# Performance work log

Hardware: AMD Instinct MI355X
Metric: run time of the kernel (lower is better)

Reference implementation:

```python
import jax, jax.numpy as jnp
import numpy as np

B, N, F, D, H, S_OBJ, S_REG, ITERS = 32, 1024, 1152, 512, 8, 8, 4, 3
S = S_OBJ + S_REG
HD = D // H
SCALE = HD ** -0.5


def ln(x, g, b, eps=1e-5):
    m = x.mean(-1, keepdims=True)
    v = ((x - m) ** 2).mean(-1, keepdims=True)
    return (x - m) / jnp.sqrt(v + eps) * g + b


def setup_inputs() -> dict:
    key = jax.random.key(0)
    ks = jax.random.split(key, 16)
    s = 0.02
    d = {
        'features': jax.random.normal(ks[0], (B, N, F), jnp.float32),
        'noise': jax.random.normal(ks[1], (B, S, D), jnp.float32),
        'w_in': jax.random.normal(ks[2], (F, D), jnp.float32) * s,
        'b_in': jnp.zeros((D,), jnp.float32),
        'ln1_g': jnp.ones((D,), jnp.float32), 'ln1_b': jnp.zeros((D,), jnp.float32),
        'slot_mu': jax.random.normal(ks[3], (1, S, D), jnp.float32) * D ** -0.5,
        'slot_log_sigma': jnp.zeros((1, S, D), jnp.float32),
        'wq': jax.random.normal(ks[4], (D, D), jnp.float32) * s,
        'wk': jax.random.normal(ks[5], (D, D), jnp.float32) * s,
        'wv': jax.random.normal(ks[6], (D, D), jnp.float32) * s,
        'gru_wih': jax.random.normal(ks[7], (D, 3 * D), jnp.float32) * s,
        'gru_whh': jax.random.normal(ks[8], (D, 3 * D), jnp.float32) * s,
        'gru_bih': jnp.zeros((3 * D,), jnp.float32),
        'gru_bhh': jnp.zeros((3 * D,), jnp.float32),
        'nslots_g': jnp.ones((D,), jnp.float32), 'nslots_b': jnp.zeros((D,), jnp.float32),
        'ninput_g': jnp.ones((D,), jnp.float32), 'ninput_b': jnp.zeros((D,), jnp.float32),
        'ffn_ln_g': jnp.ones((D,), jnp.float32), 'ffn_ln_b': jnp.zeros((D,), jnp.float32),
        'ffn_w1': jax.random.normal(ks[9], (D, 4 * D), jnp.float32) * s,
        'ffn_b1': jnp.zeros((4 * D,), jnp.float32),
        'ffn_w2': jax.random.normal(ks[10], (4 * D, D), jnp.float32) * s,
        'ffn_b2': jnp.zeros((D,), jnp.float32),
        'sel_w1': jax.random.normal(ks[11], (D, D // 2), jnp.float32) * s,
        'sel_b1': jnp.zeros((D // 2,), jnp.float32),
        'sel_w2': jax.random.normal(ks[12], (D // 2, 2), jnp.float32) * s,
        'sel_b2': jnp.zeros((2,), jnp.float32),
    }
    return d


def reference(features, noise, w_in, b_in, ln1_g, ln1_b, slot_mu, slot_log_sigma,
              wq, wk, wv, gru_wih, gru_whh, gru_bih, gru_bhh,
              nslots_g, nslots_b, ninput_g, ninput_b,
              ffn_ln_g, ffn_ln_b, ffn_w1, ffn_b1, ffn_w2, ffn_b2,
              sel_w1, sel_b1, sel_w2, sel_b2):
    b = features.shape[0]
    # input_proj: Linear + LayerNorm, then norm_input LayerNorm
    x = ln(features @ w_in + b_in, ln1_g, ln1_b)
    inp = ln(x, ninput_g, ninput_b)
    slots = slot_mu + jnp.exp(slot_log_sigma) * noise  # [B,S,D]
    k = (inp @ wk).reshape(b, N, H, HD)
    v = (inp @ wv).reshape(b, N, H, HD)
    attn_out = None
    for _ in range(ITERS):
        sn = ln(slots, nslots_g, nslots_b)
        q = (sn @ wq).reshape(b, S, H, HD)
        dots = jnp.einsum('bihd,bjhd->bihj', q, k) * SCALE  # [B,S,H,N]
        # softmax over flattened (slot, head) axis per key j
        attn = jax.nn.softmax(dots.reshape(b, S * H, N), axis=1).reshape(b, S, H, N)
        attn_out = attn.mean(axis=2)  # [B,S,N]
        attn_n = (attn + 1e-8) / (attn.sum(axis=-1, keepdims=True) + 1e-8)
        upd = jnp.einsum('bjhd,bihj->bihd', v, attn_n).reshape(b * S, D)
        h = slots.reshape(b * S, D)
        gx = upd @ gru_wih + gru_bih
        gh = h @ gru_whh + gru_bhh
        xr, xz, xn = jnp.split(gx, 3, axis=-1)
        hr, hz, hn = jnp.split(gh, 3, axis=-1)
        r = jax.nn.sigmoid(xr + hr)
        z = jax.nn.sigmoid(xz + hz)
        n = jnp.tanh(xn + r * hn)
        slots = ((1.0 - z) * n + z * h).reshape(b, S, D)
        f = ln(slots, ffn_ln_g, ffn_ln_b)
        f = jax.nn.gelu(f @ ffn_w1 + ffn_b1, approximate=False) @ ffn_w2 + ffn_b2
        slots = slots + f
    obj = slots[:, :S_OBJ]  # [B,num_slots,D]
    logits = jax.nn.relu(obj @ sel_w1 + sel_b1) @ sel_w2 + sel_b2  # [B,num_slots,2]
    decision = (jnp.argmax(logits, axis=-1) == 1).astype(slots.dtype)
    # eval-mode repair: ensure >=2 active slots per row (deterministic: first inactive)
    needed = jnp.maximum(0.0, 2.0 - decision.sum(-1, keepdims=True))
    inactive_rank = jnp.cumsum(1.0 - decision, axis=-1)
    add = ((decision == 0) & (inactive_rank <= needed)).astype(decision.dtype)
    decision = decision + add
    obj = obj * decision[..., None]
    return obj, decision, attn_out[:, :S_OBJ]
```

## Files before the change

### kernel.cpp

```cpp
#include <hip/hip_runtime.h>
#include <math.h>

typedef __attribute__((ext_vector_type(8))) short short8;
typedef __attribute__((ext_vector_type(4))) float f32x4;

typedef const __attribute__((address_space(1))) void gv_t;
typedef __attribute__((address_space(3))) void lv_t;

__device__ __forceinline__ float b2f(short u) {
  union { unsigned int i; float f; } c; c.i = ((unsigned int)(unsigned short)u) << 16; return c.f;
}
__device__ __forceinline__ short f2b(float f) {
  union { float f; unsigned int i; } c; c.f = f;
  unsigned int r = c.i + 0x7FFFu + ((c.i >> 16) & 1u);
  return (short)(r >> 16);
}
__device__ __forceinline__ void glds(const short* g, short* l) {
  __builtin_amdgcn_global_load_lds((gv_t*)g, (lv_t*)l, 16, 0, 0);
}


__global__ __launch_bounds__(256) void k_convA(const float* __restrict__ in, short* __restrict__ out, int n8) {
  int idx = blockIdx.x * 256 + threadIdx.x;
  if (idx >= n8) return;
  const float4* p = (const float4*)(in + (size_t)idx * 8);
  float4 a = p[0], b = p[1];
  short8 r;
  r[0]=f2b(a.x); r[1]=f2b(a.y); r[2]=f2b(a.z); r[3]=f2b(a.w);
  r[4]=f2b(b.x); r[5]=f2b(b.y); r[6]=f2b(b.z); r[7]=f2b(b.w);
  *(short8*)(out + (size_t)idx*8) = r;
}


__global__ __launch_bounds__(256) void k_prep(
    const float* __restrict__ w_in, const float* __restrict__ wk, const float* __restrict__ wv,
    const float* __restrict__ wq, const float* __restrict__ wih, const float* __restrict__ whh,
    const float* __restrict__ bih, const float* __restrict__ bhh,
    const float* __restrict__ w1, const float* __restrict__ w2, const float* __restrict__ sl1,
    const float* __restrict__ mu, const float* __restrict__ lsig, const float* __restrict__ noise,
    short* __restrict__ Bt1, short* __restrict__ Btkv, short* __restrict__ wq_t,
    short* __restrict__ wgru, float* __restrict__ gbias,
    short* __restrict__ w1_t, short* __restrict__ w2_t, short* __restrict__ sl1_t,
    float* __restrict__ slots, short* __restrict__ gruA)
{
  int blk = blockIdx.x, t = threadIdx.x;
  if (blk < 2304) {
    int idx = blk*256 + t;
    int kk = idx / 512, n = idx % 512;
    Bt1[(size_t)n*1152 + kk] = f2b(w_in[idx]);
  } else if (blk < 4352) {
    int idx = (blk-2304)*256 + t;
    int kk = idx >> 10, n = idx & 1023;
    float v = (n < 512) ? wk[kk*512 + n] : wv[kk*512 + (n-512)];
    Btkv[(size_t)n*512 + kk] = f2b(v);
  } else if (blk < 5376) {
    int idx = (blk-4352)*256 + t;
    int kk = idx >> 9, n = idx & 511;
    wq_t[n*512 + kk] = f2b(wq[idx]);
  } else if (blk < 13568) {
    int idx = (blk-5376)*256 + t;
    int n = idx >> 10, k = idx & 1023;
    int g = n >> 9, c = n & 511;
    float v;
    if (g == 0)      v = (k < 512) ? wih[k*1536 + c]        : whh[(k-512)*1536 + c];
    else if (g == 1) v = (k < 512) ? wih[k*1536 + 512 + c]  : whh[(k-512)*1536 + 512 + c];
    else if (g == 2) v = (k < 512) ? wih[k*1536 + 1024 + c] : 0.f;
    else             v = (k < 512) ? 0.f                    : whh[(k-512)*1536 + 1024 + c];
    wgru[(size_t)n*1024 + k] = f2b(v);
  } else if (blk < 17664) {
    int idx = (blk-13568)*256 + t;
    int kk = idx >> 11, n = idx & 2047;
    w1_t[(size_t)n*512 + kk] = f2b(w1[idx]);
  } else if (blk < 21760) {
    int idx = (blk-17664)*256 + t;
    int kk = idx >> 9, n = idx & 511;
    w2_t[(size_t)n*2048 + kk] = f2b(w2[idx]);
  } else if (blk < 22272) {
    int idx = (blk-21760)*256 + t;
    int kk = idx >> 8, n = idx & 255;
    sl1_t[n*512 + kk] = f2b(sl1[idx]);
  } else if (blk < 22280) {
    int n = (blk-22272)*256 + t;
    int g = n >> 9;
    float v;
    if (g <= 1)      v = bih[n] + bhh[n];
    else if (g == 2) v = bih[n];
    else             v = bhh[1024 + (n - 1536)];
    gbias[n] = v;
  } else {
    int idx = (blk-22280)*256 + t;
    int sd = idx % 6144;
    float v = mu[sd] + __expf(lsig[sd]) * noise[idx];
    slots[idx] = v;
    int row = idx >> 9, c = idx & 511;
    gruA[(size_t)row*1024 + 512 + c] = f2b(v);
  }
}


__global__ __launch_bounds__(256) void gemm_p(
    const short* __restrict__ A, const short* __restrict__ Bt,
    const float* __restrict__ bias, short* __restrict__ Cb,
    int N, int K, int lda, int ldb)
{
  __shared__ short As[2][128*64];
  __shared__ short Bs[2][128*64];
  const int t = threadIdx.x;
  const int lane = t & 63, wave = t >> 6;

  const int nwg = gridDim.x, gridX = N >> 7, orig = blockIdx.x;
  const int q = nwg >> 3, r = nwg & 7, xcd = orig & 7, base = orig >> 3;
  const int wgid = (xcd < r ? xcd*(q+1) : r*(q+1) + (xcd - r)*q) + base;
  const int bx = wgid % gridX, by = wgid / gridX;

  const int rowBase = by * 128, colBase = bx * 128;
  const int wm = (wave >> 1) * 64, wn = (wave & 1) * 64;
  const int fr = lane & 15, kcf = lane >> 4;
  f32x4 acc[4][4] = {};

  int srow[4], scol[4];
  #pragma unroll
  for (int i = 0; i < 4; ++i) {
    int c = i*256 + t;
    srow[i] = c >> 3;
    scol[i] = ((c & 7) ^ (srow[i] & 7)) * 8;
  }

  const int nsteps = K >> 6;
  auto STAGE = [&](int step, int buf) {
    int kb = step * 64;
    #pragma unroll
    for (int i = 0; i < 4; ++i) {
      int c = i*256 + t;
      glds(A + (size_t)(rowBase + srow[i])*lda + kb + scol[i], As[buf] + c*8);
      glds(Bt + (size_t)(colBase + srow[i])*ldb + kb + scol[i], Bs[buf] + c*8);
    }
  };

  STAGE(0, 0);
  if (nsteps > 1) { STAGE(1, 1); asm volatile("s_waitcnt vmcnt(8)" ::: "memory"); }
  else            {              asm volatile("s_waitcnt vmcnt(0)" ::: "memory"); }
  __builtin_amdgcn_sched_barrier(0);
  __builtin_amdgcn_s_barrier();
  __builtin_amdgcn_sched_barrier(0);

  for (int tt = 0; tt < nsteps; ++tt) {
    const int cur = tt & 1;
    short8 af[2][4], bf[2][4];
    #pragma unroll
    for (int ks = 0; ks < 2; ++ks) {
      int kc = ks*4 + kcf;
      #pragma unroll
      for (int m = 0; m < 4; ++m) {
        int rowa = wm + m*16 + fr;
        af[ks][m] = *(const short8*)(As[cur] + rowa*64 + (kc ^ (rowa & 7))*8);
        int rowb = wn + m*16 + fr;
        bf[ks][m] = *(const short8*)(Bs[cur] + rowb*64 + (kc ^ (rowb & 7))*8);
      }
    }
    asm volatile("s_waitcnt lgkmcnt(0)" ::: "memory");
    __builtin_amdgcn_sched_barrier(0);
    __builtin_amdgcn_s_barrier();
    __builtin_amdgcn_sched_barrier(0);
    if (tt + 2 < nsteps) STAGE(tt + 2, cur);
    #pragma unroll
    for (int ks = 0; ks < 2; ++ks)
      #pragma unroll
      for (int m = 0; m < 4; ++m)
        #pragma unroll
        for (int n = 0; n < 4; ++n)
          acc[m][n] = __builtin_amdgcn_mfma_f32_16x16x32_bf16(af[ks][m], bf[ks][n], acc[m][n], 0, 0, 0);
    if (tt + 1 < nsteps) {
      if (tt + 2 < nsteps) asm volatile("s_waitcnt vmcnt(8)" ::: "memory");
      else                 asm volatile("s_waitcnt vmcnt(0)" ::: "memory");
      __builtin_amdgcn_sched_barrier(0);
      __builtin_amdgcn_s_barrier();
      __builtin_amdgcn_sched_barrier(0);
    }
  }

  const int cr = (lane >> 4) * 4, cc2 = lane & 15;
  #pragma unroll
  for (int m = 0; m < 4; ++m)
    #pragma unroll
    for (int n = 0; n < 4; ++n) {
      int col = colBase + wn + n*16 + cc2;
      float bv = bias ? bias[col] : 0.f;
      #pragma unroll
      for (int j = 0; j < 4; ++j) {
        int row = rowBase + wm + m*16 + cr + j;
        Cb[(size_t)row*N + col] = f2b(acc[m][n][j] + bv);
      }
    }
}


template<int ACT, bool OUTBF, bool SPLITK>
__global__ __launch_bounds__(256) void gemm_t(
    const short* __restrict__ A, const short* __restrict__ Bt,
    const float* __restrict__ bias,
    float* __restrict__ Cf, short* __restrict__ Cb,
    int N, int Kp, int lda, int ldb, int ldf, int ldcb, int cboff, int skstride)
{
  __shared__ short As[128*64];
  __shared__ short Bs[128*64];
  const int t = threadIdx.x;
  const int lane = t & 63, wave = t >> 6;

  const int nwg = gridDim.x, gridX = N >> 7, orig = blockIdx.x;
  const int q = nwg >> 3, r = nwg & 7, xcd = orig & 7, base = orig >> 3;
  const int wgid = (xcd < r ? xcd*(q+1) : r*(q+1) + (xcd - r)*q) + base;
  const int bx = wgid % gridX, by = wgid / gridX;

  const int rowBase = by * 128, colBase = bx * 128;
  const size_t koff = (size_t)blockIdx.y * Kp;
  const int wm = (wave >> 1) * 64, wn = (wave & 1) * 64;
  const int fr = lane & 15, kcf = lane >> 4;
  f32x4 acc[4][4] = {};

  int srow[4], scol[4];
  #pragma unroll
  for (int i = 0; i < 4; ++i) {
    int c = i*256 + t;
    srow[i] = c >> 3;
    scol[i] = ((c & 7) ^ (srow[i] & 7)) * 8;
  }

  for (int kb = 0; kb < Kp; kb += 64) {
    __syncthreads();
    #pragma unroll
    for (int i = 0; i < 4; ++i) {
      int c = i*256 + t;
      glds(A + (size_t)(rowBase + srow[i])*lda + koff + kb + scol[i], As + c*8);
      glds(Bt + (size_t)(colBase + srow[i])*ldb + koff + kb + scol[i], Bs + c*8);
    }
    __syncthreads();
    #pragma unroll
    for (int ks = 0; ks < 2; ++ks) {
      short8 af[4], bf[4];
      #pragma unroll
      for (int m = 0; m < 4; ++m) {
        int row = wm + m*16 + fr;
        int kc = ks*4 + kcf;
        af[m] = *(const short8*)(As + row*64 + (kc ^ (row & 7))*8);
      }
      #pragma unroll
      for (int n = 0; n < 4; ++n) {
        int row = wn + n*16 + fr;
        int kc = ks*4 + kcf;
        bf[n] = *(const short8*)(Bs + row*64 + (kc ^ (row & 7))*8);
      }
      #pragma unroll
      for (int m = 0; m < 4; ++m)
        #pragma unroll
        for (int n = 0; n < 4; ++n)
          acc[m][n] = __builtin_amdgcn_mfma_f32_16x16x32_bf16(af[m], bf[n], acc[m][n], 0, 0, 0);
    }
  }

  const int cr = (lane >> 4) * 4, cc2 = lane & 15;
  if (SPLITK) {
    float* dst = Cf + (size_t)blockIdx.y * skstride;
    #pragma unroll
    for (int m = 0; m < 4; ++m)
      #pragma unroll
      for (int n = 0; n < 4; ++n) {
        int col = colBase + wn + n*16 + cc2;
        #pragma unroll
        for (int j = 0; j < 4; ++j) {
          int row = rowBase + wm + m*16 + cr + j;
          dst[(size_t)row * ldf + col] = acc[m][n][j];
        }
      }
  } else {
    #pragma unroll
    for (int m = 0; m < 4; ++m)
      #pragma unroll
      for (int n = 0; n < 4; ++n) {
        int col = colBase + wn + n*16 + cc2;
        float bv = bias ? bias[col] : 0.f;
        #pragma unroll
        for (int j = 0; j < 4; ++j) {
          int row = rowBase + wm + m*16 + cr + j;
          float v = acc[m][n][j] + bv;
          if (ACT == 1) v = 0.5f*v*(1.f + erff(v*0.70710678118f));
          else if (ACT == 2) v = fmaxf(v, 0.f);
          if (OUTBF) Cb[(size_t)row*ldcb + cboff + col] = f2b(v);
          else Cf[(size_t)row*ldf + col] = v;
        }
      }
  }
}


__global__ __launch_bounds__(256) void k_gruact_sk(const float* __restrict__ p, const float* __restrict__ gbias,
                                                   float* __restrict__ slots)
{
  int idx = blockIdx.x*256 + threadIdx.x;
  int row = idx >> 9, c = idx & 511;
  const float* base = p + (size_t)row*2048 + c;
  float g0=gbias[c], g1=gbias[512+c], g2=gbias[1024+c], g3=gbias[1536+c];
  #pragma unroll
  for (int s = 0; s < 4; ++s) {
    const float* qq = base + (size_t)s*786432;
    g0 += qq[0]; g1 += qq[512]; g2 += qq[1024]; g3 += qq[1536];
  }
  float r = 1.f/(1.f+__expf(-g0));
  float z = 1.f/(1.f+__expf(-g1));
  float n = tanhf(g2 + r*g3);
  slots[idx] = (1.f-z)*n + z*slots[idx];
}

__global__ __launch_bounds__(256) void k_ffn1red(const float* __restrict__ p, const float* __restrict__ b1,
                                                 short* __restrict__ f1) {
  int i = blockIdx.x*256 + threadIdx.x;
  int col = (i*8) & 2047;
  float v[8], w[8];
  *(float4*)v = *(const float4*)(p + (size_t)i*8);
  *(float4*)(v+4) = *(const float4*)(p + (size_t)i*8 + 4);
  const float* p2 = p + 786432;
  *(float4*)w = *(const float4*)(p2 + (size_t)i*8);
  *(float4*)(w+4) = *(const float4*)(p2 + (size_t)i*8 + 4);
  short8 o;
  #pragma unroll
  for (int e = 0; e < 8; ++e) {
    float x = v[e] + w[e] + b1[col + e];
    x = 0.5f*x*(1.f + erff(x*0.70710678118f));
    o[e] = f2b(x);
  }
  *(short8*)(f1 + (size_t)i*8) = o;
}

__global__ __launch_bounds__(256) void k_ffn2red(const float* __restrict__ p, const float* __restrict__ b2,
                                                 float* __restrict__ slots, short* __restrict__ gruA) {
  int i = blockIdx.x*256 + threadIdx.x;
  int base = i*8;
  int row = base >> 9, c = base & 511;
  float v[8] = {0.f,0.f,0.f,0.f,0.f,0.f,0.f,0.f};
  #pragma unroll
  for (int s = 0; s < 8; ++s) {
    const float* qq = p + (size_t)s*196608 + base;
    float4 a = *(const float4*)qq, b = *(const float4*)(qq+4);
    v[0]+=a.x; v[1]+=a.y; v[2]+=a.z; v[3]+=a.w;
    v[4]+=b.x; v[5]+=b.y; v[6]+=b.z; v[7]+=b.w;
  }
  float sl[8];
  *(float4*)sl = *(const float4*)(slots + base);
  *(float4*)(sl+4) = *(const float4*)(slots + base + 4);
  short8 o;
  #pragma unroll
  for (int e = 0; e < 8; ++e) {
    float ns = sl[e] + v[e] + b2[c+e];
    sl[e] = ns;
    o[e] = f2b(ns);
  }
  *(float4*)(slots + base) = *(float4*)sl;
  *(float4*)(slots + base + 4) = *(float4*)(sl+4);
  *(short8*)(gruA + (size_t)row*1024 + 512 + c) = o;
}


__global__ __launch_bounds__(256) void k_ln2(const short* __restrict__ y, short* __restrict__ inp,
    const float* __restrict__ g1, const float* __restrict__ b1,
    const float* __restrict__ g2, const float* __restrict__ b2)
{
  int t = threadIdx.x, lane = t & 63;
  int row = blockIdx.x * 4 + (t >> 6);
  const short8 raw = *(const short8*)(y + (size_t)row*512 + lane*8);
  float x[8];
  #pragma unroll
  for (int e = 0; e < 8; ++e) x[e] = b2f(raw[e]);
  float s = 0.f, ss = 0.f;
  #pragma unroll
  for (int e = 0; e < 8; ++e) { s += x[e]; ss += x[e]*x[e]; }
  #pragma unroll
  for (int m = 1; m < 64; m <<= 1) { s += __shfl_xor(s, m, 64); ss += __shfl_xor(ss, m, 64); }
  float mean = s * (1.f/512.f);
  float rs = rsqrtf(ss*(1.f/512.f) - mean*mean + 1e-5f);
  int c = lane * 8;
  #pragma unroll
  for (int e = 0; e < 8; ++e) x[e] = (x[e]-mean)*rs*g1[c+e] + b1[c+e];
  s = 0.f; ss = 0.f;
  #pragma unroll
  for (int e = 0; e < 8; ++e) { s += x[e]; ss += x[e]*x[e]; }
  #pragma unroll
  for (int m = 1; m < 64; m <<= 1) { s += __shfl_xor(s, m, 64); ss += __shfl_xor(ss, m, 64); }
  float mean2 = s * (1.f/512.f);
  float rs2 = rsqrtf(ss*(1.f/512.f) - mean2*mean2 + 1e-5f);
  short8 o;
  #pragma unroll
  for (int e = 0; e < 8; ++e) o[e] = f2b((x[e]-mean2)*rs2*g2[c+e] + b2[c+e]);
  *(short8*)(inp + (size_t)row*512 + lane*8) = o;
}


__global__ __launch_bounds__(256) void k_lnb(const float* __restrict__ x, short* __restrict__ out,
    const float* __restrict__ g, const float* __restrict__ b)
{
  int t = threadIdx.x, lane = t & 63;
  int row = blockIdx.x * 4 + (t >> 6);
  const float* src = x + (size_t)row*512 + lane*8;
  float v[8];
  *(float4*)v = *(const float4*)src;
  *(float4*)(v+4) = *(const float4*)(src+4);
  float s = 0.f, ss = 0.f;
  #pragma unroll
  for (int e = 0; e < 8; ++e) { s += v[e]; ss += v[e]*v[e]; }
  #pragma unroll
  for (int m = 1; m < 64; m <<= 1) { s += __shfl_xor(s, m, 64); ss += __shfl_xor(ss, m, 64); }
  float mean = s * (1.f/512.f);
  float rs = rsqrtf(ss*(1.f/512.f) - mean*mean + 1e-5f);
  int c = lane * 8;
  short8 o;
  #pragma unroll
  for (int e = 0; e < 8; ++e) o[e] = f2b((v[e]-mean)*rs*g[c+e] + b[c+e]);
  *(short8*)(out + (size_t)row*512 + c) = o;
}


__global__ __launch_bounds__(256) void k_attn(
    const float* __restrict__ qparts, const short* __restrict__ kv,
    float* __restrict__ pvp, float* __restrict__ denp, float* __restrict__ aout)
{
  __shared__ float qs[12][512];
  __shared__ float ksh[128][65];
  __shared__ float dots[96][132];
  const int t = threadIdx.x;
  const int jt = blockIdx.x, b = blockIdx.y;

  for (int i = t; i < 6144; i += 256) {
    int s = i >> 9, d = i & 511;
    size_t o = (size_t)(b*12+s)*512 + d;
    qs[s][d] = qparts[o] + qparts[196608 + o] + qparts[393216 + o] + qparts[589824 + o];
  }

  const int jj = t & 127, sg = t >> 7;
  for (int h = 0; h < 8; ++h) {
    __syncthreads();
    #pragma unroll
    for (int i = 0; i < 4; ++i) {
      int c = i*256 + t;
      int j2 = c >> 3, seg = (c & 7) * 8;
      short8 raw = *(const short8*)(kv + ((size_t)(b*1024 + jt*128 + j2))*1024 + h*64 + seg);
      #pragma unroll
      for (int e = 0; e < 8; ++e) ksh[j2][seg+e] = b2f(raw[e]);
    }
    __syncthreads();
    float d6[6] = {};
    for (int d = 0; d < 64; ++d) {
      float kvv = ksh[jj][d];
      #pragma unroll
      for (int i = 0; i < 6; ++i) d6[i] += qs[sg*6+i][h*64+d] * kvv;
    }
    #pragma unroll
    for (int i = 0; i < 6; ++i) dots[(sg*6+i)*8 + h][jj] = d6[i] * 0.125f;
  }
  __syncthreads();

  {
    int j = t >> 1, half = (t & 1) * 48;
    float mx = -1e30f;
    #pragma unroll
    for (int i = 0; i < 48; ++i) mx = fmaxf(mx, dots[half+i][j]);
    mx = fmaxf(mx, __shfl_xor(mx, 1, 64));
    float ex[48];
    float sum = 0.f;
    #pragma unroll
    for (int i = 0; i < 48; ++i) { ex[i] = __expf(dots[half+i][j] - mx); sum += ex[i]; }
    sum += __shfl_xor(sum, 1, 64);
    float inv = 1.f / sum;
    float as_[6] = {0,0,0,0,0,0};
    #pragma unroll
    for (int i = 0; i < 48; ++i) {
      float a = ex[i] * inv;
      dots[half+i][j] = a;
      as_[i >> 3] += a;
    }
    if (aout) {
      int sbase = (t & 1) * 6;
      #pragma unroll
      for (int q2 = 0; q2 < 6; ++q2) {
        int s = sbase + q2;
        if (s < 8) aout[((size_t)(b*8+s))*1024 + jt*128 + j] = as_[q2] * 0.125f;
      }
    }
  }

  const int d = t & 63, sq = t >> 6;
  for (int h = 0; h < 8; ++h) {
    __syncthreads();
    #pragma unroll
    for (int i = 0; i < 4; ++i) {
      int c = i*256 + t;
      int j2 = c >> 3, seg = (c & 7) * 8;
      short8 raw = *(const short8*)(kv + ((size_t)(b*1024 + jt*128 + j2))*1024 + 512 + h*64 + seg);
      #pragma unroll
      for (int e = 0; e < 8; ++e) ksh[j2][seg+e] = b2f(raw[e]);
    }
    __syncthreads();
    float a3[3] = {0.f, 0.f, 0.f};
    for (int j2 = 0; j2 < 128; ++j2) {
      float vv = ksh[j2][d];
      #pragma unroll
      for (int i = 0; i < 3; ++i) a3[i] += dots[(sq + 4*i)*8 + h][j2] * vv;
    }
    #pragma unroll
    for (int i = 0; i < 3; ++i)
      pvp[((size_t)(jt*32+b))*6144 + (sq + 4*i)*512 + h*64 + d] = a3[i];
    if (t < 12) {
      float ls = 0.f;
      for (int j2 = 0; j2 < 128; ++j2) ls += dots[t*8 + h][j2];
      denp[((size_t)(jt*32+b))*96 + t*8 + h] = ls;
    }
  }
}


__global__ __launch_bounds__(256) void k_pvred(const float* __restrict__ pvp, const float* __restrict__ denp,
                                               short* __restrict__ gruA)
{
  __shared__ float den[96];
  int t = threadIdx.x, b = blockIdx.x;
  if (t < 96) {
    float s = 0.f;
    #pragma unroll
    for (int jt2 = 0; jt2 < 8; ++jt2) s += denp[((size_t)(jt2*32+b))*96 + t];
    den[t] = s + 1e-8f;
  }
  __syncthreads();
  for (int i = t; i < 6144; i += 256) {
    int s = i >> 9, rem = i & 511, h = rem >> 6;
    float acc = 0.f;
    #pragma unroll
    for (int jt2 = 0; jt2 < 8; ++jt2) acc += pvp[((size_t)(jt2*32+b))*6144 + i];
    gruA[((size_t)(b*12+s))*1024 + rem] = f2b(acc / den[s*8 + h]);
  }
}


__global__ __launch_bounds__(64) void k_decide(const float* __restrict__ hid, const float* __restrict__ w2,
    const float* __restrict__ b2, const float* __restrict__ slots, float* __restrict__ out)
{
  __shared__ float lg[16];
  __shared__ float dec[8];
  int b = blockIdx.x, t = threadIdx.x;
  if (t < 16) {
    int s = t >> 1, cl = t & 1;
    const float* hr = hid + (size_t)(b*12+s)*256;
    float a = b2[cl];
    for (int k = 0; k < 256; ++k) a += hr[k] * w2[k*2+cl];
    lg[t] = a;
  }
  __syncthreads();
  if (t == 0) {
    float d0[8]; float tot = 0.f;
    #pragma unroll
    for (int s = 0; s < 8; ++s) { d0[s] = (lg[2*s+1] > lg[2*s]) ? 1.f : 0.f; tot += d0[s]; }
    float needed = fmaxf(0.f, 2.f - tot);
    float cum = 0.f;
    #pragma unroll
    for (int s = 0; s < 8; ++s) {
      cum += 1.f - d0[s];
      float add = (d0[s] == 0.f && cum <= needed) ? 1.f : 0.f;
      float dd = d0[s] + add;
      dec[s] = dd;
      out[131072 + b*8 + s] = dd;
    }
  }
  __syncthreads();
  for (int i = 0; i < 64; ++i) {
    int idx = i*64 + t;
    int s = idx >> 9, c = idx & 511;
    out[(size_t)(b*8+s)*512 + c] = slots[(size_t)(b*12+s)*512 + c] * dec[s];
  }
}


extern "C" void kernel_launch(void* const* d_in, const int* in_sizes, int n_in,
                              void* d_out, int out_size, void* d_ws, size_t ws_size,
                              hipStream_t stream) {
  const float* features = (const float*)d_in[0];
  const float* noise    = (const float*)d_in[1];
  const float* w_in     = (const float*)d_in[2];
  const float* b_in     = (const float*)d_in[3];
  const float* ln1_g    = (const float*)d_in[4];
  const float* ln1_b    = (const float*)d_in[5];
  const float* slot_mu  = (const float*)d_in[6];
  const float* slot_ls  = (const float*)d_in[7];
  const float* wq       = (const float*)d_in[8];
  const float* wk       = (const float*)d_in[9];
  const float* wv       = (const float*)d_in[10];
  const float* gru_wih  = (const float*)d_in[11];
  const float* gru_whh  = (const float*)d_in[12];
  const float* gru_bih  = (const float*)d_in[13];
  const float* gru_bhh  = (const float*)d_in[14];
  const float* nslots_g = (const float*)d_in[15];
  const float* nslots_b = (const float*)d_in[16];
  const float* ninput_g = (const float*)d_in[17];
  const float* ninput_b = (const float*)d_in[18];
  const float* ffnln_g  = (const float*)d_in[19];
  const float* ffnln_b  = (const float*)d_in[20];
  const float* ffn_w1   = (const float*)d_in[21];
  const float* ffn_b1   = (const float*)d_in[22];
  const float* ffn_w2   = (const float*)d_in[23];
  const float* ffn_b2   = (const float*)d_in[24];
  const float* sel_w1   = (const float*)d_in[25];
  const float* sel_b1   = (const float*)d_in[26];
  const float* sel_w2   = (const float*)d_in[27];
  const float* sel_b2   = (const float*)d_in[28];
  float* out = (float*)d_out;
  float* fnull = (float*)nullptr;
  short* snull = (short*)nullptr;

  char* w = (char*)d_ws;
  size_t off = 0;
  auto alloc = [&](size_t n) { char* p = w + off; off = (off + n + 255) & ~255ULL; return p; };
  short* Abf   = (short*)alloc(75497472);
  short* kv    = Abf;
  short* ybf   = (short*)alloc(33554432);
  short* inp   = (short*)alloc(33554432);
  short* Bt1   = (short*)alloc(1179648);
  short* Btkv  = (short*)alloc(1048576);
  short* wq_t  = (short*)alloc(524288);
  short* wgru  = (short*)alloc(4194304);
  float* gbias = (float*)alloc(8192);
  short* w1_t  = (short*)alloc(2097152);
  short* w2_t  = (short*)alloc(2097152);
  short* sl1_t = (short*)alloc(262144);
  float* slots = (float*)alloc(786432);
  short* gruA  = (short*)alloc(786432);
  short* sn    = (short*)alloc(393216);
  float* parts = (float*)alloc(12582912);
  float* pvp   = (float*)alloc(6291456);
  float* denp  = (float*)alloc(98304);
  short* fln   = (short*)alloc(393216);
  short* f1    = (short*)alloc(1572864);
  float* hid   = (float*)alloc(393216);
  (void)ws_size; (void)in_sizes; (void)n_in; (void)out_size;

  k_convA<<<dim3(18432), dim3(256), 0, stream>>>(features, Abf, 4718592);
  k_prep<<<dim3(23048), dim3(256), 0, stream>>>(
      w_in, wk, wv, wq, gru_wih, gru_whh, gru_bih, gru_bhh,
      ffn_w1, ffn_w2, sel_w1, slot_mu, slot_ls, noise,
      Bt1, Btkv, wq_t, wgru, gbias, w1_t, w2_t, sl1_t, slots, gruA);

  gemm_p<<<dim3(1024), dim3(256), 0, stream>>>(Abf, Bt1, b_in, ybf, 512, 1152, 1152, 1152);
  k_ln2<<<dim3(8192), dim3(256), 0, stream>>>(ybf, inp, ln1_g, ln1_b, ninput_g, ninput_b);
  gemm_p<<<dim3(2048), dim3(256), 0, stream>>>(inp, Btkv, fnull, kv, 1024, 512, 512, 512);

  for (int it = 0; it < 3; ++it) {
    k_lnb<<<dim3(96), dim3(256), 0, stream>>>(slots, sn, nslots_g, nslots_b);
    gemm_t<0,false,true><<<dim3(12, 4), dim3(256), 0, stream>>>(
        sn, wq_t, fnull, parts, snull, 512, 128, 512, 512, 512, 0, 0, 196608);
    k_attn<<<dim3(8, 32), dim3(256), 0, stream>>>(parts, kv, pvp, denp,
        it == 2 ? out + 131328 : fnull);
    k_pvred<<<dim3(32), dim3(256), 0, stream>>>(pvp, denp, gruA);
    gemm_t<0,false,true><<<dim3(48, 4), dim3(256), 0, stream>>>(
        gruA, wgru, fnull, parts, snull, 2048, 256, 1024, 1024, 2048, 0, 0, 786432);
    k_gruact_sk<<<dim3(768), dim3(256), 0, stream>>>(parts, gbias, slots);
    k_lnb<<<dim3(96), dim3(256), 0, stream>>>(slots, fln, ffnln_g, ffnln_b);
    gemm_t<0,false,true><<<dim3(48, 2), dim3(256), 0, stream>>>(
        fln, w1_t, fnull, parts, snull, 2048, 256, 512, 512, 2048, 0, 0, 786432);
    k_ffn1red<<<dim3(384), dim3(256), 0, stream>>>(parts, ffn_b1, f1);
    gemm_t<0,false,true><<<dim3(12, 8), dim3(256), 0, stream>>>(
        f1, w2_t, fnull, parts, snull, 512, 256, 2048, 2048, 512, 0, 0, 196608);
    k_ffn2red<<<dim3(96), dim3(256), 0, stream>>>(parts, ffn_b2, slots, gruA);
  }

  gemm_t<2,false,false><<<dim3(6), dim3(256), 0, stream>>>(
      gruA + 512, sl1_t, sel_b1, hid, snull, 256, 512, 1024, 512, 256, 0, 0, 0);
  k_decide<<<dim3(32), dim3(64), 0, stream>>>(hid, sel_w2, sel_b2, slots, out);
}
```

Before: 551.7 us.

## Fuse fp32-to-bf16 conversion into input GEMM and fuse LayerNorms into reductions

Removes the standalone conversion kernel by adding a GEMM variant that stages fp32 features directly into LDS and converts them to bf16 in registers just before the MFMA. It also fuses the GRU activation with the following FFN LayerNorm, and the FFN2 reduction with the next iteration's slot LayerNorm, which removes per-iteration launches. The intent is to avoid writing and re-reading a large bf16 copy of the features, at the cost of doubling the A-tile LDS traffic in the input GEMM and adding conversion ALU work inside its loop.

```diff
diff --git a/kernel.cpp b/kernel.cpp
--- a/kernel.cpp
+++ b/kernel.cpp
@@ -15,20 +15,17 @@
   unsigned int r = c.i + 0x7FFFu + ((c.i >> 16) & 1u);
   return (short)(r >> 16);
 }
-__device__ __forceinline__ void glds(const short* g, short* l) {
-  __builtin_amdgcn_global_load_lds((gv_t*)g, (lv_t*)l, 16, 0, 0);
-}
-
-
-__global__ __launch_bounds__(256) void k_convA(const float* __restrict__ in, short* __restrict__ out, int n8) {
-  int idx = blockIdx.x * 256 + threadIdx.x;
-  if (idx >= n8) return;
-  const float4* p = (const float4*)(in + (size_t)idx * 8);
-  float4 a = p[0], b = p[1];
+__device__ __forceinline__ short8 cvt8(float4 a, float4 b) {
   short8 r;
   r[0]=f2b(a.x); r[1]=f2b(a.y); r[2]=f2b(a.z); r[3]=f2b(a.w);
   r[4]=f2b(b.x); r[5]=f2b(b.y); r[6]=f2b(b.z); r[7]=f2b(b.w);
-  *(short8*)(out + (size_t)idx*8) = r;
+  return r;
+}
+__device__ __forceinline__ void glds(const short* g, short* l) {
+  __builtin_amdgcn_global_load_lds((gv_t*)g, (lv_t*)l, 16, 0, 0);
+}
+__device__ __forceinline__ void gldsf(const float* g, float* l) {
+  __builtin_amdgcn_global_load_lds((gv_t*)g, (lv_t*)l, 16, 0, 0);
 }
 
 
@@ -98,6 +95,113 @@
 }
 
 
+__global__ __launch_bounds__(256) void gemm_p32(
+    const float* __restrict__ A, const short* __restrict__ Bt,
+    const float* __restrict__ bias, short* __restrict__ Cb,
+    int N, int K, int lda, int ldb)
+{
+  __shared__ float As[2][128*32];
+  __shared__ short Bs[2][128*32];
+  const int t = threadIdx.x;
+  const int lane = t & 63, wave = t >> 6;
+
+  const int nwg = gridDim.x, gridX = N >> 7, orig = blockIdx.x;
+  const int q = nwg >> 3, r = nwg & 7, xcd = orig & 7, base = orig >> 3;
+  const int wgid = (xcd < r ? xcd*(q+1) : r*(q+1) + (xcd - r)*q) + base;
+  const int bx = wgid % gridX, by = wgid / gridX;
+
+  const int rowBase = by * 128, colBase = bx * 128;
+  const int wm = (wave >> 1) * 64, wn = (wave & 1) * 64;
+  const int fr = lane & 15, kcf = lane >> 4;
+  f32x4 acc[4][4] = {};
+
+  int arow[4], acol[4];
+  #pragma unroll
+  for (int i = 0; i < 4; ++i) {
+    int c = i*256 + t;
+    arow[i] = c >> 3;
+    acol[i] = ((c & 7) ^ (arow[i] & 7)) * 4;
+  }
+  int brow[2], bcol[2];
+  #pragma unroll
+  for (int i = 0; i < 2; ++i) {
+    int c = i*256 + t;
+    brow[i] = c >> 2;
+    bcol[i] = ((c & 3) ^ (brow[i] & 3)) * 8;
+  }
+
+  const int nsteps = K >> 5;
+  auto STAGE = [&](int step, int buf) {
+    int kb = step * 32;
+    #pragma unroll
+    for (int i = 0; i < 4; ++i)
+      gldsf(A + (size_t)(rowBase + arow[i])*lda + kb + acol[i], As[buf] + (i*256+t)*4);
+    #pragma unroll
+    for (int i = 0; i < 2; ++i)
+      glds(Bt + (size_t)(colBase + brow[i])*ldb + kb + bcol[i], Bs[buf] + (i*256+t)*8);
+  };
+
+  STAGE(0, 0);
+  if (nsteps > 1) { STAGE(1, 1); asm volatile("s_waitcnt vmcnt(6)" ::: "memory"); }
+  else            {              asm volatile("s_waitcnt vmcnt(0)" ::: "memory"); }
+  __builtin_amdgcn_sched_barrier(0);
+  __builtin_amdgcn_s_barrier();
+  __builtin_amdgcn_sched_barrier(0);
+
+  for (int tt = 0; tt < nsteps; ++tt) {
+    const int cur = tt & 1;
+    float4 ar[4][2];
+    short8 bf[4];
+    #pragma unroll
+    for (int m = 0; m < 4; ++m) {
+      int ra = wm + m*16 + fr;
+      const float* Ar = As[cur] + ra*32;
+      ar[m][0] = *(const float4*)(Ar + ((2*kcf)   ^ (ra & 7))*4);
+      ar[m][1] = *(const float4*)(Ar + ((2*kcf+1) ^ (ra & 7))*4);
+    }
+    #pragma unroll
+    for (int n = 0; n < 4; ++n) {
+      int rb = wn + n*16 + fr;
+      bf[n] = *(const short8*)(Bs[cur] + rb*32 + (kcf ^ (rb & 3))*8);
+    }
+    asm volatile("s_waitcnt lgkmcnt(0)" ::: "memory");
+    __builtin_amdgcn_sched_barrier(0);
+    __builtin_amdgcn_s_barrier();
+    __builtin_amdgcn_sched_barrier(0);
+    if (tt + 2 < nsteps) STAGE(tt + 2, cur);
+    short8 af[4];
+    #pragma unroll
+    for (int m = 0; m < 4; ++m) af[m] = cvt8(ar[m][0], ar[m][1]);
+    #pragma unroll
+    for (int m = 0; m < 4; ++m)
+      #pragma unroll
+      for (int n = 0; n < 4; ++n)
+        acc[m][n] = __builtin_amdgcn_mfma_f32_16x16x32_bf16(af[m], bf[n], acc[m][n], 0, 0, 0);
+    if (tt + 1 < nsteps) {
+      if (tt + 2 < nsteps) asm volatile("s_waitcnt vmcnt(6)" ::: "memory");
+      else                 asm volatile("s_waitcnt vmcnt(0)" ::: "memory");
+      __builtin_amdgcn_sched_barrier(0);
+      __builtin_amdgcn_s_barrier();
+      __builtin_amdgcn_sched_barrier(0);
+    }
+  }
+
+  const int cr = (lane >> 4) * 4, cc2 = lane & 15;
+  #pragma unroll
+  for (int m = 0; m < 4; ++m)
+    #pragma unroll
+    for (int n = 0; n < 4; ++n) {
+      int col = colBase + wn + n*16 + cc2;
+      float bv = bias ? bias[col] : 0.f;
+      #pragma unroll
+      for (int j = 0; j < 4; ++j) {
+        int row = rowBase + wm + m*16 + cr + j;
+        Cb[(size_t)row*N + col] = f2b(acc[m][n][j] + bv);
+      }
+    }
+}
+
+
 __global__ __launch_bounds__(256) void gemm_p(
     const short* __restrict__ A, const short* __restrict__ Bt,
     const float* __restrict__ bias, short* __restrict__ Cb,
@@ -293,23 +397,86 @@
 }
 
 
-__global__ __launch_bounds__(256) void k_gruact_sk(const float* __restrict__ p, const float* __restrict__ gbias,
-                                                   float* __restrict__ slots)
-{
-  int idx = blockIdx.x*256 + threadIdx.x;
-  int row = idx >> 9, c = idx & 511;
-  const float* base = p + (size_t)row*2048 + c;
-  float g0=gbias[c], g1=gbias[512+c], g2=gbias[1024+c], g3=gbias[1536+c];
-  #pragma unroll
-  for (int s = 0; s < 4; ++s) {
-    const float* qq = base + (size_t)s*786432;
-    g0 += qq[0]; g1 += qq[512]; g2 += qq[1024]; g3 += qq[1536];
-  }
-  float r = 1.f/(1.f+__expf(-g0));
-  float z = 1.f/(1.f+__expf(-g1));
-  float n = tanhf(g2 + r*g3);
-  slots[idx] = (1.f-z)*n + z*slots[idx];
-}
+__global__ __launch_bounds__(256) void k_gruln(const float* __restrict__ p, const float* __restrict__ gbias,
+    float* __restrict__ slots, short* __restrict__ fln,
+    const float* __restrict__ g, const float* __restrict__ bb)
+{
+  int t = threadIdx.x, lane = t & 63;
+  int row = blockIdx.x*4 + (t >> 6);
+  int c = lane * 8;
+  float hold[8], v[8];
+  *(float4*)hold     = *(const float4*)(slots + (size_t)row*512 + c);
+  *(float4*)(hold+4) = *(const float4*)(slots + (size_t)row*512 + c + 4);
+  const float* base = p + (size_t)row*2048;
+  #pragma unroll
+  for (int e = 0; e < 8; ++e) {
+    int cc = c + e;
+    float g0=gbias[cc], g1=gbias[512+cc], g2=gbias[1024+cc], g3=gbias[1536+cc];
+    #pragma unroll
+    for (int s = 0; s < 4; ++s) {
+      const float* qq = base + (size_t)s*786432 + cc;
+      g0 += qq[0]; g1 += qq[512]; g2 += qq[1024]; g3 += qq[1536];
+    }
+    float r = 1.f/(1.f+__expf(-g0));
+    float z = 1.f/(1.f+__expf(-g1));
+    float n = tanhf(g2 + r*g3);
+    v[e] = (1.f-z)*n + z*hold[e];
+  }
+  *(float4*)(slots + (size_t)row*512 + c)     = *(float4*)v;
+  *(float4*)(slots + (size_t)row*512 + c + 4) = *(float4*)(v+4);
+  float s1 = 0.f, s2 = 0.f;
+  #pragma unroll
+  for (int e = 0; e < 8; ++e) { s1 += v[e]; s2 += v[e]*v[e]; }
+  #pragma unroll
+  for (int m = 1; m < 64; m <<= 1) { s1 += __shfl_xor(s1, m, 64); s2 += __shfl_xor(s2, m, 64); }
+  float mean = s1 * (1.f/512.f);
+  float rs = rsqrtf(s2*(1.f/512.f) - mean*mean + 1e-5f);
+  short8 o;
+  #pragma unroll
+  for (int e = 0; e < 8; ++e) o[e] = f2b((v[e]-mean)*rs*g[c+e] + bb[c+e]);
+  *(short8*)(fln + (size_t)row*512 + c) = o;
+}
+
+
+__global__ __launch_bounds__(256) void k_ffn2redln(const float* __restrict__ p, const float* __restrict__ b2,
+    float* __restrict__ slots, short* __restrict__ gruA, short* __restrict__ sn,
+    const float* __restrict__ g, const float* __restrict__ bb)
+{
+  int t = threadIdx.x, lane = t & 63;
+  int row = blockIdx.x*4 + (t >> 6);
+  int c = lane * 8;
+  size_t base = (size_t)row*512 + c;
+  float v[8];
+  *(float4*)v     = *(const float4*)(slots + base);
+  *(float4*)(v+4) = *(const float4*)(slots + base + 4);
+  #pragma unroll
+  for (int e = 0; e < 8; ++e) v[e] += b2[c+e];
+  #pragma unroll
+  for (int s = 0; s < 8; ++s) {
+    const float* qq = p + (size_t)s*196608 + base;
+    float4 a = *(const float4*)qq, b4 = *(const float4*)(qq+4);
+    v[0]+=a.x; v[1]+=a.y; v[2]+=a.z; v[3]+=a.w;
+    v[4]+=b4.x; v[5]+=b4.y; v[6]+=b4.z; v[7]+=b4.w;
+  }
+  *(float4*)(slots + base)     = *(float4*)v;
+  *(float4*)(slots + base + 4) = *(float4*)(v+4);
+  short8 o;
+  #pragma unroll
+  for (int e = 0; e < 8; ++e) o[e] = f2b(v[e]);
+  *(short8*)(gruA + (size_t)row*1024 + 512 + c) = o;
+  float s1 = 0.f, s2 = 0.f;
+  #pragma unroll
+  for (int e = 0; e < 8; ++e) { s1 += v[e]; s2 += v[e]*v[e]; }
+  #pragma unroll
+  for (int m = 1; m < 64; m <<= 1) { s1 += __shfl_xor(s1, m, 64); s2 += __shfl_xor(s2, m, 64); }
+  float mean = s1 * (1.f/512.f);
+  float rs = rsqrtf(s2*(1.f/512.f) - mean*mean + 1e-5f);
+  short8 o2;
+  #pragma unroll
+  for (int e = 0; e < 8; ++e) o2[e] = f2b((v[e]-mean)*rs*g[c+e] + bb[c+e]);
+  *(short8*)(sn + base) = o2;
+}
+
 
 __global__ __launch_bounds__(256) void k_ffn1red(const float* __restrict__ p, const float* __restrict__ b1,
                                                  short* __restrict__ f1) {
@@ -329,34 +496,6 @@
     o[e] = f2b(x);
   }
   *(short8*)(f1 + (size_t)i*8) = o;
-}
-
-__global__ __launch_bounds__(256) void k_ffn2red(const float* __restrict__ p, const float* __restrict__ b2,
-                                                 float* __restrict__ slots, short* __restrict__ gruA) {
-  int i = blockIdx.x*256 + threadIdx.x;
-  int base = i*8;
-  int row = base >> 9, c = base & 511;
-  float v[8] = {0.f,0.f,0.f,0.f,0.f,0.f,0.f,0.f};
-  #pragma unroll
-  for (int s = 0; s < 8; ++s) {
-    const float* qq = p + (size_t)s*196608 + base;
-    float4 a = *(const float4*)qq, b = *(const float4*)(qq+4);
-    v[0]+=a.x; v[1]+=a.y; v[2]+=a.z; v[3]+=a.w;
-    v[4]+=b.x; v[5]+=b.y; v[6]+=b.z; v[7]+=b.w;
-  }
-  float sl[8];
-  *(float4*)sl = *(const float4*)(slots + base);
-  *(float4*)(sl+4) = *(const float4*)(slots + base + 4);
-  short8 o;
-  #pragma unroll
-  for (int e = 0; e < 8; ++e) {
-    float ns = sl[e] + v[e] + b2[c+e];
-    sl[e] = ns;
-    o[e] = f2b(ns);
-  }
-  *(float4*)(slots + base) = *(float4*)sl;
-  *(float4*)(slots + base + 4) = *(float4*)(sl+4);
-  *(short8*)(gruA + (size_t)row*1024 + 512 + c) = o;
 }
 
 
@@ -615,8 +754,7 @@
   char* w = (char*)d_ws;
   size_t off = 0;
   auto alloc = [&](size_t n) { char* p = w + off; off = (off + n + 255) & ~255ULL; return p; };
-  short* Abf   = (short*)alloc(75497472);
-  short* kv    = Abf;
+  short* kv    = (short*)alloc(67108864);
   short* ybf   = (short*)alloc(33554432);
   short* inp   = (short*)alloc(33554432);
   short* Bt1   = (short*)alloc(1179648);
@@ -638,18 +776,18 @@
   float* hid   = (float*)alloc(393216);
   (void)ws_size; (void)in_sizes; (void)n_in; (void)out_size;
 
-  k_convA<<<dim3(18432), dim3(256), 0, stream>>>(features, Abf, 4718592);
   k_prep<<<dim3(23048), dim3(256), 0, stream>>>(
       w_in, wk, wv, wq, gru_wih, gru_whh, gru_bih, gru_bhh,
       ffn_w1, ffn_w2, sel_w1, slot_mu, slot_ls, noise,
       Bt1, Btkv, wq_t, wgru, gbias, w1_t, w2_t, sl1_t, slots, gruA);
 
-  gemm_p<<<dim3(1024), dim3(256), 0, stream>>>(Abf, Bt1, b_in, ybf, 512, 1152, 1152, 1152);
+  gemm_p32<<<dim3(1024), dim3(256), 0, stream>>>(features, Bt1, b_in, ybf, 512, 1152, 1152, 1152);
   k_ln2<<<dim3(8192), dim3(256), 0, stream>>>(ybf, inp, ln1_g, ln1_b, ninput_g, ninput_b);
   gemm_p<<<dim3(2048), dim3(256), 0, stream>>>(inp, Btkv, fnull, kv, 1024, 512, 512, 512);
 
+  k_lnb<<<dim3(96), dim3(256), 0, stream>>>(slots, sn, nslots_g, nslots_b);
+
   for (int it = 0; it < 3; ++it) {
-    k_lnb<<<dim3(96), dim3(256), 0, stream>>>(slots, sn, nslots_g, nslots_b);
     gemm_t<0,false,true><<<dim3(12, 4), dim3(256), 0, stream>>>(
         sn, wq_t, fnull, parts, snull, 512, 128, 512, 512, 512, 0, 0, 196608);
     k_attn<<<dim3(8, 32), dim3(256), 0, stream>>>(parts, kv, pvp, denp,
@@ -657,14 +795,14 @@
     k_pvred<<<dim3(32), dim3(256), 0, stream>>>(pvp, denp, gruA);
     gemm_t<0,false,true><<<dim3(48, 4), dim3(256), 0, stream>>>(
         gruA, wgru, fnull, parts, snull, 2048, 256, 1024, 1024, 2048, 0, 0, 786432);
-    k_gruact_sk<<<dim3(768), dim3(256), 0, stream>>>(parts, gbias, slots);
-    k_lnb<<<dim3(96), dim3(256), 0, stream>>>(slots, fln, ffnln_g, ffnln_b);
+    k_gruln<<<dim3(96), dim3(256), 0, stream>>>(parts, gbias, slots, fln, ffnln_g, ffnln_b);
     gemm_t<0,false,true><<<dim3(48, 2), dim3(256), 0, stream>>>(
         fln, w1_t, fnull, parts, snull, 2048, 256, 512, 512, 2048, 0, 0, 786432);
     k_ffn1red<<<dim3(384), dim3(256), 0, stream>>>(parts, ffn_b1, f1);
     gemm_t<0,false,true><<<dim3(12, 8), dim3(256), 0, stream>>>(
         f1, w2_t, fnull, parts, snull, 512, 256, 2048, 2048, 512, 0, 0, 196608);
-    k_ffn2red<<<dim3(96), dim3(256), 0, stream>>>(parts, ffn_b2, slots, gruA);
+    k_ffn2redln<<<dim3(96), dim3(256), 0, stream>>>(parts, ffn_b2, slots, gruA, sn,
+        nslots_g, nslots_b);
   }
 
   gemm_t<2,false,false><<<dim3(6), dim3(256), 0, stream>>>(
```

New measurement: 597.5 us. 1.08x slower.
